# Kernel tuning notes

Measured on AMD Instinct MI355X. Metric: run time of the kernel, lower is better.

Reference implementation:

```python
import jax, jax.numpy as jnp
import numpy as np

B, N, E, HID, ED, NH = 2, 10000, 160000, 128, 32, 8
HD = HID // NH  # head_dim = 16
EPS = 1e-5


def setup_inputs() -> dict:
    key = jax.random.key(0)
    ks = jax.random.split(key, 12)
    s = 0.05  # keep pre-tanh activations in a sane range
    return {
        "h": jax.random.normal(ks[0], (B, N, HID), jnp.float32),
        "edge_attr": jax.random.normal(ks[1], (B, E, ED), jnp.float32),
        "edge_index": jax.random.randint(ks[2], (E, 2), 0, N),
        "Wq": jax.random.normal(ks[3], (HID, HID), jnp.float32) * s,
        "bq": jnp.zeros((HID,), jnp.float32),
        "Wk": jax.random.normal(ks[4], (HID, HID), jnp.float32) * s,
        "bk": jnp.zeros((HID,), jnp.float32),
        "Wv": jax.random.normal(ks[5], (HID, HID), jnp.float32) * s,
        "bv": jnp.zeros((HID,), jnp.float32),
        "We": jax.random.normal(ks[6], (HID, ED), jnp.float32) * s,
        "be": jnp.zeros((HID,), jnp.float32),
        "attn_vec": jax.random.normal(ks[7], (NH, HD), jnp.float32) * 0.02,
        "Ws": jax.random.normal(ks[8], (HID, HID), jnp.float32) * s,
        "bs": jnp.zeros((HID,), jnp.float32),
        "Wa": jax.random.normal(ks[9], (HID, HID), jnp.float32) * s,
        "ba": jnp.zeros((HID,), jnp.float32),
        "ln_g": jnp.ones((HID,), jnp.float32),
        "ln_b": jnp.zeros((HID,), jnp.float32),
    }


def reference(h, edge_attr, edge_index, Wq, bq, Wk, bk, Wv, bv, We, be,
              attn_vec, Ws, bs, Wa, ba, ln_g, ln_b):
    src = edge_index[:, 0]
    dst = edge_index[:, 1]
    b, n, hid = h.shape
    e_cnt = src.shape[0]

    h_src = h[:, src, :]  # [B,E,HID]
    h_dst = h[:, dst, :]

    q = (h_dst @ Wq.T + bq).reshape(b, e_cnt, NH, HD)
    k = (h_src @ Wk.T + bk).reshape(b, e_cnt, NH, HD)
    v = (h_src @ Wv.T + bv).reshape(b, e_cnt, NH, HD)
    e = (edge_attr @ We.T + be).reshape(b, e_cnt, NH, HD)

    # GATv2-style scores: [B,E,NH]
    logits = jnp.einsum('behd,hd->beh', jnp.tanh(q + k + e), attn_vec)
    logits = logits / np.float32(np.sqrt(HD))

    # segment softmax over edges grouped by dst node (stable)
    lt = jnp.transpose(logits, (1, 0, 2))  # [E,B,NH]
    mx = jax.ops.segment_max(lt, dst, num_segments=n)  # [N,B,NH]
    ex = jnp.exp(lt - mx[dst])
    den = jax.ops.segment_sum(ex, dst, num_segments=n)
    alpha = jnp.transpose(ex / den[dst], (1, 0, 2))  # [B,E,NH]

    msg = (alpha[..., None] * (v + e)).reshape(b, e_cnt, hid)  # [B,E,HID]
    agg = jax.ops.segment_sum(jnp.transpose(msg, (1, 0, 2)), dst, num_segments=n)
    agg = jnp.transpose(agg, (1, 0, 2))  # [B,N,HID]

    update = (h @ Ws.T + bs) + (agg @ Wa.T + ba)
    x = h + jax.nn.gelu(update, approximate=False)  # dropout is identity in eval

    mu = jnp.mean(x, axis=-1, keepdims=True)
    var = jnp.var(x, axis=-1, keepdims=True)
    return (x - mu) / jnp.sqrt(var + EPS) * ln_g + ln_b
```

## Files before the change

kernel.cpp:

```cpp
#include <hip/hip_runtime.h>
#include <math.h>
#include <stdint.h>

#define B_   2
#define N_   10000
#define E_   160000
#define HID_ 128
#define ED_  32
#define NH_  8
#define HD_  16
#define ROWS_ (B_ * N_)

using half2_t = __attribute__((ext_vector_type(2))) _Float16;

__device__ __forceinline__ half2_t f2h2(float a, float b) {
    return __builtin_bit_cast(half2_t, __builtin_amdgcn_cvt_pkrtz(a, b));
}
__device__ __forceinline__ uint32_t pkh2(float a, float b) {
    return __builtin_bit_cast(uint32_t, __builtin_amdgcn_cvt_pkrtz(a, b));
}


__global__ void zero_kernel(int* __restrict__ deg, int* __restrict__ cursor, int n) {
    int i = blockIdx.x * 256 + threadIdx.x;
    if (i < n) { deg[i] = 0; cursor[i] = 0; }
}

__global__ void hist_kernel(const int* __restrict__ ei, int* __restrict__ deg, int E) {
    int e = blockIdx.x * 256 + threadIdx.x;
    if (e < E) atomicAdd(&deg[ei[2 * e + 1]], 1);
}

__global__ __launch_bounds__(256) void scan_kernel(const int* __restrict__ deg,
                                                   int* __restrict__ off, int N) {
    __shared__ int sums[256];
    int t = threadIdx.x;
    int chunk = (N + 255) / 256;
    int s0 = t * chunk, s1 = min(N, s0 + chunk);
    int s = 0;
    for (int i = s0; i < s1; ++i) s += deg[i];
    sums[t] = s;
    __syncthreads();
    if (t == 0) {
        int run = 0;
        for (int i = 0; i < 256; ++i) { int v = sums[i]; sums[i] = run; run += v; }
        off[N] = run;
    }
    __syncthreads();
    int run = sums[t];
    for (int i = s0; i < s1; ++i) { off[i] = run; run += deg[i]; }
}

__global__ void fill_kernel(const int* __restrict__ ei, const int* __restrict__ off,
                            int* __restrict__ cursor, int* __restrict__ csr, int E) {
    int e = blockIdx.x * 256 + threadIdx.x;
    if (e < E) {
        int d = ei[2 * e + 1];
        int p = atomicAdd(&cursor[d], 1);
        csr[off[d] + p] = e;
    }
}


#define R_T 32
#define JC2 64
#define LDH2 68

__global__ __launch_bounds__(256) void qkvs_kernel(
    const float* __restrict__ h,
    const float* __restrict__ Wq, const float* __restrict__ bq,
    const float* __restrict__ Wk, const float* __restrict__ bk,
    const float* __restrict__ Wv, const float* __restrict__ bv,
    const float* __restrict__ Ws, const float* __restrict__ bs,
    const float* __restrict__ ba,
    float* __restrict__ Q, float* __restrict__ KV, float* __restrict__ S)
{
    __shared__ uint32_t hs[R_T * LDH2];
    __shared__ uint32_t wsm[JC2 * LDH2];
    __shared__ float bsm[512];

    int tid = threadIdx.x;
    int row0 = blockIdx.x * R_T;

    for (int f = tid; f < 512; f += 256) {
        float v;
        if (f < 128) v = bq[f];
        else if (f < 256) v = bk[f - 128];
        else if (f < 384) v = bv[f - 256];
        else v = bs[f - 384] + ba[f - 384];
        bsm[f] = v;
    }

    for (int f = tid; f < R_T * 32; f += 256) {
        int r = f >> 5, c4 = f & 31;
        float4 hv = *(const float4*)(h + (long)(row0 + r) * HID_ + c4 * 4);
        hs[r * LDH2 + c4 * 2]     = pkh2(hv.x, hv.y);
        hs[r * LDH2 + c4 * 2 + 1] = pkh2(hv.z, hv.w);
    }

    int rg = tid & 15;
    int cg = tid >> 4;

    for (int jc = 0; jc < 8; ++jc) {
        __syncthreads();
        for (int f = tid; f < JC2 * 32; f += 256) {
            int jr = f >> 5, c4 = f & 31;
            int J = jc * JC2 + jr;
            const float* Wp;
            if (J < 128)      Wp = Wq + (long)J * HID_;
            else if (J < 256) Wp = Wk + (long)(J - 128) * HID_;
            else if (J < 384) Wp = Wv + (long)(J - 256) * HID_;
            else              Wp = Ws + (long)(J - 384) * HID_;
            float4 wv = *(const float4*)(Wp + c4 * 4);
            wsm[jr * LDH2 + c4 * 2]     = pkh2(wv.x, wv.y);
            wsm[jr * LDH2 + c4 * 2 + 1] = pkh2(wv.z, wv.w);
        }
        __syncthreads();

        float acc[2][4];
        #pragma unroll
        for (int r = 0; r < 2; ++r)
            #pragma unroll
            for (int m = 0; m < 4; ++m) acc[r][m] = 0.f;

        #pragma unroll 4
        for (int kk = 0; kk < 16; ++kk) {
            const half2_t* h0 = (const half2_t*)(hs + rg * LDH2 + kk * 4);
            const half2_t* h1 = (const half2_t*)(hs + (rg + 16) * LDH2 + kk * 4);
            const half2_t* w0 = (const half2_t*)(wsm + cg * LDH2 + kk * 4);
            const half2_t* w1 = (const half2_t*)(wsm + (cg + 16) * LDH2 + kk * 4);
            const half2_t* w2 = (const half2_t*)(wsm + (cg + 32) * LDH2 + kk * 4);
            const half2_t* w3 = (const half2_t*)(wsm + (cg + 48) * LDH2 + kk * 4);
            #pragma unroll
            for (int d = 0; d < 4; ++d) {
                half2_t a0 = h0[d], a1 = h1[d];
                half2_t b0 = w0[d], b1 = w1[d], b2 = w2[d], b3 = w3[d];
                acc[0][0] = __builtin_amdgcn_fdot2(a0, b0, acc[0][0], false);
                acc[0][1] = __builtin_amdgcn_fdot2(a0, b1, acc[0][1], false);
                acc[0][2] = __builtin_amdgcn_fdot2(a0, b2, acc[0][2], false);
                acc[0][3] = __builtin_amdgcn_fdot2(a0, b3, acc[0][3], false);
                acc[1][0] = __builtin_amdgcn_fdot2(a1, b0, acc[1][0], false);
                acc[1][1] = __builtin_amdgcn_fdot2(a1, b1, acc[1][1], false);
                acc[1][2] = __builtin_amdgcn_fdot2(a1, b2, acc[1][2], false);
                acc[1][3] = __builtin_amdgcn_fdot2(a1, b3, acc[1][3], false);
            }
        }

        #pragma unroll
        for (int r = 0; r < 2; ++r) {
            long row = row0 + rg + r * 16;
            #pragma unroll
            for (int m = 0; m < 4; ++m) {
                int J = jc * JC2 + cg + m * 16;
                float v = acc[r][m] + bsm[J];
                if (J < 128)      Q[row * 128 + J] = v;
                else if (J < 256) KV[row * 256 + 2 * (J - 128)] = v;
                else if (J < 384) KV[row * 256 + 2 * (J - 256) + 1] = v;
                else              S[row * 128 + (J - 384)] = v;
            }
        }
    }
}

__global__ __launch_bounds__(256) void wa_kernel(
    const float* __restrict__ X, const float* __restrict__ Wa, float* __restrict__ A)
{
    __shared__ uint32_t hs[R_T * LDH2];
    __shared__ uint32_t wsm[JC2 * LDH2];

    int tid = threadIdx.x;
    int row0 = blockIdx.x * R_T;

    for (int f = tid; f < R_T * 32; f += 256) {
        int r = f >> 5, c4 = f & 31;
        float4 hv = *(const float4*)(X + (long)(row0 + r) * HID_ + c4 * 4);
        hs[r * LDH2 + c4 * 2]     = pkh2(hv.x, hv.y);
        hs[r * LDH2 + c4 * 2 + 1] = pkh2(hv.z, hv.w);
    }

    int rg = tid & 15;
    int cg = tid >> 4;

    for (int jc = 0; jc < 2; ++jc) {
        __syncthreads();
        for (int f = tid; f < JC2 * 32; f += 256) {
            int jr = f >> 5, c4 = f & 31;
            int J = jc * JC2 + jr;
            float4 wv = *(const float4*)(Wa + (long)J * HID_ + c4 * 4);
            wsm[jr * LDH2 + c4 * 2]     = pkh2(wv.x, wv.y);
            wsm[jr * LDH2 + c4 * 2 + 1] = pkh2(wv.z, wv.w);
        }
        __syncthreads();

        float acc[2][4];
        #pragma unroll
        for (int r = 0; r < 2; ++r)
            #pragma unroll
            for (int m = 0; m < 4; ++m) acc[r][m] = 0.f;

        #pragma unroll 4
        for (int kk = 0; kk < 16; ++kk) {
            const half2_t* h0 = (const half2_t*)(hs + rg * LDH2 + kk * 4);
            const half2_t* h1 = (const half2_t*)(hs + (rg + 16) * LDH2 + kk * 4);
            const half2_t* w0 = (const half2_t*)(wsm + cg * LDH2 + kk * 4);
            const half2_t* w1 = (const half2_t*)(wsm + (cg + 16) * LDH2 + kk * 4);
            const half2_t* w2 = (const half2_t*)(wsm + (cg + 32) * LDH2 + kk * 4);
            const half2_t* w3 = (const half2_t*)(wsm + (cg + 48) * LDH2 + kk * 4);
            #pragma unroll
            for (int d = 0; d < 4; ++d) {
                half2_t a0 = h0[d], a1 = h1[d];
                half2_t b0 = w0[d], b1 = w1[d], b2 = w2[d], b3 = w3[d];
                acc[0][0] = __builtin_amdgcn_fdot2(a0, b0, acc[0][0], false);
                acc[0][1] = __builtin_amdgcn_fdot2(a0, b1, acc[0][1], false);
                acc[0][2] = __builtin_amdgcn_fdot2(a0, b2, acc[0][2], false);
                acc[0][3] = __builtin_amdgcn_fdot2(a0, b3, acc[0][3], false);
                acc[1][0] = __builtin_amdgcn_fdot2(a1, b0, acc[1][0], false);
                acc[1][1] = __builtin_amdgcn_fdot2(a1, b1, acc[1][1], false);
                acc[1][2] = __builtin_amdgcn_fdot2(a1, b2, acc[1][2], false);
                acc[1][3] = __builtin_amdgcn_fdot2(a1, b3, acc[1][3], false);
            }
        }

        #pragma unroll
        for (int r = 0; r < 2; ++r) {
            long row = row0 + rg + r * 16;
            #pragma unroll
            for (int m = 0; m < 4; ++m) {
                int J = jc * JC2 + cg + m * 16;
                A[row * 128 + J] = acc[r][m];
            }
        }
    }
}


template <int CTRL>
__device__ __forceinline__ float dpp_add(float x) {
    int y = __builtin_amdgcn_mov_dpp(__float_as_int(x), CTRL, 0xF, 0xF, true);
    return x + __int_as_float(y);
}
__device__ __forceinline__ float hsum16(float p) {
    p = dpp_add<0xB1>(p);
    p = dpp_add<0x4E>(p);
    p = dpp_add<0x141>(p);
    p = dpp_add<0x140>(p);
    return p;
}


#define NPB 4
#define CHUNK 96
#define EAS 20

__global__ __launch_bounds__(128) void node_kernel(
    const float* __restrict__ edge_attr, const int* __restrict__ ei,
    const float* __restrict__ Q, const float* __restrict__ KV,
    const float* __restrict__ We, const float* __restrict__ be,
    const float* __restrict__ attn_vec,
    const int* __restrict__ off, const int* __restrict__ csr,
    float* __restrict__ agg)
{
    int n0 = blockIdx.x * NPB;
    int b  = blockIdx.y;
    int j  = threadIdx.x;
    long bN = (long)b * N_;

    __shared__ int sL[CHUNK];
    __shared__ uint32_t eaL[CHUNK * EAS];

    half2_t we16[16];
    {
        const float4* We4 = (const float4*)(We + (long)j * ED_);
        #pragma unroll
        for (int c = 0; c < 8; ++c) {
            float4 w = We4[c];
            we16[2 * c]     = f2h2(w.x, w.y);
            we16[2 * c + 1] = f2h2(w.z, w.w);
        }
    }
    float bej = be[j];
    float avj = attn_vec[j];

    float q0 = Q[(bN + n0 + 0) * 128 + j];
    float q1 = Q[(bN + n0 + 1) * 128 + j];
    float q2 = Q[(bN + n0 + 2) * 128 + j];
    float q3 = Q[(bN + n0 + 3) * 128 + j];

    int o0 = off[n0];
    int c1 = off[n0 + 1] - o0, c2 = off[n0 + 2] - o0,
        c3 = off[n0 + 3] - o0, c4_ = off[n0 + 4] - o0;
    int total = c4_;

    const float* eab = edge_attr + (long)b * E_ * ED_;
    const float* KVb = KV + bN * 256;

    float acc0 = 0.f, den0 = 0.f, acc1 = 0.f, den1 = 0.f;
    float acc2 = 0.f, den2 = 0.f, acc3 = 0.f, den3 = 0.f;

    auto edge_body = [&](int i, float qg, float& accg, float& deng) {
        int s = sL[i];
        float2 kv = *(const float2*)(KVb + (long)s * 256 + 2 * j);
        float ej = bej;
        const half2_t* ea = (const half2_t*)(eaL + i * EAS);
        #pragma unroll
        for (int c = 0; c < 16; ++c)
            ej = __builtin_amdgcn_fdot2(we16[c], ea[c], ej, false);
        float y = qg + kv.x + ej;
        float t = 1.f - 2.f * __builtin_amdgcn_rcpf(__expf(2.f * y) + 1.f);
        float p = hsum16(t * avj);
        float ex = __expf(p * 0.25f);
        deng += ex;
        accg += ex * (kv.y + ej);
    };

    auto range_loop = [&](int lo, int hi, float qg, float& accg, float& deng) {
        int i = lo;
        for (; i + 3 < hi; i += 4) {
            edge_body(i, qg, accg, deng);
            edge_body(i + 1, qg, accg, deng);
            edge_body(i + 2, qg, accg, deng);
            edge_body(i + 3, qg, accg, deng);
        }
        for (; i < hi; ++i) edge_body(i, qg, accg, deng);
    };

    for (int tau = 0; tau < total; tau += CHUNK) {
        int rows = min(total - tau, CHUNK);
        __syncthreads();
        for (int t = j; t < rows; t += 128) {
            int e = csr[o0 + tau + t];
            sL[t] = ei[2 * e];
        }
        for (int idx = j; idx < rows * 8; idx += 128) {
            int r = idx >> 3, c = idx & 7;
            int e = csr[o0 + tau + r];
            float4 f = *(const float4*)(eab + (long)e * ED_ + c * 4);
            eaL[r * EAS + c * 2]     = pkh2(f.x, f.y);
            eaL[r * EAS + c * 2 + 1] = pkh2(f.z, f.w);
        }
        __syncthreads();

        range_loop(max(0 - tau, 0),   min(c1 - tau, rows), q0, acc0, den0);
        range_loop(max(c1 - tau, 0),  min(c2 - tau, rows), q1, acc1, den1);
        range_loop(max(c2 - tau, 0),  min(c3 - tau, rows), q2, acc2, den2);
        range_loop(max(c3 - tau, 0),  min(c4_ - tau, rows), q3, acc3, den3);
    }

    agg[(bN + n0 + 0) * 128 + j] = (c1 > 0)   ? acc0 * __builtin_amdgcn_rcpf(den0) : 0.f;
    agg[(bN + n0 + 1) * 128 + j] = (c2 > c1)  ? acc1 * __builtin_amdgcn_rcpf(den1) : 0.f;
    agg[(bN + n0 + 2) * 128 + j] = (c3 > c2)  ? acc2 * __builtin_amdgcn_rcpf(den2) : 0.f;
    agg[(bN + n0 + 3) * 128 + j] = (c4_ > c3) ? acc3 * __builtin_amdgcn_rcpf(den3) : 0.f;
}


__global__ __launch_bounds__(128) void final_kernel(
    const float* __restrict__ h, const float* __restrict__ S, const float* __restrict__ A,
    const float* __restrict__ ln_g, const float* __restrict__ ln_b,
    float* __restrict__ out)
{
    long row = blockIdx.x;
    int j = threadIdx.x;
    __shared__ float red[4];

    float upd = S[row * 128 + j] + A[row * 128 + j];
    float ge = 0.5f * upd * (1.f + erff(upd * 0.70710678118654752f));
    float x = h[row * 128 + j] + ge;

    float s = x, s2 = x * x;
    #pragma unroll
    for (int m = 1; m < 64; m <<= 1) { s += __shfl_xor(s, m); s2 += __shfl_xor(s2, m); }
    int wv = j >> 6;
    if ((j & 63) == 0) { red[wv] = s; red[2 + wv] = s2; }
    __syncthreads();
    float Sm = red[0] + red[1], S2m = red[2] + red[3];
    float mu = Sm * (1.f / 128.f);
    float var = S2m * (1.f / 128.f) - mu * mu;
    out[row * 128 + j] = (x - mu) * rsqrtf(var + 1e-5f) * ln_g[j] + ln_b[j];
}


extern "C" void kernel_launch(void* const* d_in, const int* in_sizes, int n_in,
                              void* d_out, int out_size, void* d_ws, size_t ws_size,
                              hipStream_t stream) {
    const float* h         = (const float*)d_in[0];
    const float* edge_attr = (const float*)d_in[1];
    const int*   ei        = (const int*)  d_in[2];
    const float* Wq = (const float*)d_in[3];
    const float* bq = (const float*)d_in[4];
    const float* Wk = (const float*)d_in[5];
    const float* bk = (const float*)d_in[6];
    const float* Wv = (const float*)d_in[7];
    const float* bv = (const float*)d_in[8];
    const float* We = (const float*)d_in[9];
    const float* be = (const float*)d_in[10];
    const float* attn_vec = (const float*)d_in[11];
    const float* Ws = (const float*)d_in[12];
    const float* bs = (const float*)d_in[13];
    const float* Wa = (const float*)d_in[14];
    const float* ba = (const float*)d_in[15];
    const float* ln_g = (const float*)d_in[16];
    const float* ln_b = (const float*)d_in[17];
    float* out = (float*)d_out;

    size_t p = 0;
    auto alloc = [&](size_t bytes) { size_t r = p; p += (bytes + 255) & ~(size_t)255; return r; };
    char* ws = (char*)d_ws;
    float* Q    = (float*)(ws + alloc((size_t)ROWS_ * 128 * 4));
    float* KV   = (float*)(ws + alloc((size_t)ROWS_ * 256 * 4));
    float* S    = (float*)(ws + alloc((size_t)ROWS_ * 128 * 4));
    float* agg  = (float*)(ws + alloc((size_t)ROWS_ * 128 * 4));
    int* deg    = (int*)(ws + alloc((size_t)N_ * 4));
    int* cursor = (int*)(ws + alloc((size_t)N_ * 4));
    int* off    = (int*)(ws + alloc((size_t)(N_ + 1) * 4));
    int* csr    = (int*)(ws + alloc((size_t)E_ * 4));
    float* A = Q;
    (void)ws_size;

    zero_kernel<<<(N_ + 255) / 256, 256, 0, stream>>>(deg, cursor, N_);
    hist_kernel<<<(E_ + 255) / 256, 256, 0, stream>>>(ei, deg, E_);
    scan_kernel<<<1, 256, 0, stream>>>(deg, off, N_);
    fill_kernel<<<(E_ + 255) / 256, 256, 0, stream>>>(ei, off, cursor, csr, E_);

    qkvs_kernel<<<ROWS_ / R_T, 256, 0, stream>>>(h, Wq, bq, Wk, bk, Wv, bv, Ws, bs, ba,
                                                 Q, KV, S);

    dim3 grid(N_ / NPB, B_);
    node_kernel<<<grid, 128, 0, stream>>>(edge_attr, ei, Q, KV, We, be, attn_vec,
                                          off, csr, agg);

    wa_kernel<<<ROWS_ / R_T, 256, 0, stream>>>(agg, Wa, A);

    final_kernel<<<ROWS_, 128, 0, stream>>>(h, S, A, ln_g, ln_b, out);
}
```

Measured before the change: 206.1 us.

## Compute edge-attr projection per chunk with MFMA into shared memory

```diff
diff --git a/kernel.cpp b/kernel.cpp
--- a/kernel.cpp
+++ b/kernel.cpp
@@ -12,6 +12,8 @@
 #define ROWS_ (B_ * N_)
 
 using half2_t = __attribute__((ext_vector_type(2))) _Float16;
+using f16x8   = __attribute__((ext_vector_type(8))) _Float16;
+using f32x4   = __attribute__((ext_vector_type(4))) float;
 
 __device__ __forceinline__ half2_t f2h2(float a, float b) {
     return __builtin_bit_cast(half2_t, __builtin_amdgcn_cvt_pkrtz(a, b));
@@ -249,8 +251,9 @@
 
 
 #define NPB 4
-#define CHUNK 96
+#define CHUNK 64
 #define EAS 20
+#define PSTR 132
 
 __global__ __launch_bounds__(128) void node_kernel(
     const float* __restrict__ edge_attr, const int* __restrict__ ei,
@@ -263,22 +266,33 @@
     int n0 = blockIdx.x * NPB;
     int b  = blockIdx.y;
     int j  = threadIdx.x;
+    int lane = j & 63;
+    int wv = j >> 6;
     long bN = (long)b * N_;
 
     __shared__ int sL[CHUNK];
-    __shared__ uint32_t eaL[CHUNK * EAS];
-
-    half2_t we16[16];
+    __shared__ uint32_t eaF[CHUNK * EAS];
+    __shared__ _Float16 P16[CHUNK * PSTR];
+
+    f16x8 bfr[8];
+    float beC[8];
     {
-        const float4* We4 = (const float4*)(We + (long)j * ED_);
-        #pragma unroll
-        for (int c = 0; c < 8; ++c) {
-            float4 w = We4[c];
-            we16[2 * c]     = f2h2(w.x, w.y);
-            we16[2 * c + 1] = f2h2(w.z, w.w);
-        }
-    }
-    float bej = be[j];
+        int wrow = lane & 15;
+        int k0 = (lane >> 4) * 8;
+        #pragma unroll
+        for (int nt = 0; nt < 8; ++nt) {
+            const float* Wr = We + (long)(nt * 16 + wrow) * ED_ + k0;
+            float4 w0 = *(const float4*)(Wr);
+            float4 w1 = *(const float4*)(Wr + 4);
+            union { f16x8 v; uint32_t u[4]; } bu;
+            bu.u[0] = pkh2(w0.x, w0.y);
+            bu.u[1] = pkh2(w0.z, w0.w);
+            bu.u[2] = pkh2(w1.x, w1.y);
+            bu.u[3] = pkh2(w1.z, w1.w);
+            bfr[nt] = bu.v;
+            beC[nt] = be[nt * 16 + wrow];
+        }
+    }
     float avj = attn_vec[j];
 
     float q0 = Q[(bN + n0 + 0) * 128 + j];
@@ -300,11 +314,7 @@
     auto edge_body = [&](int i, float qg, float& accg, float& deng) {
         int s = sL[i];
         float2 kv = *(const float2*)(KVb + (long)s * 256 + 2 * j);
-        float ej = bej;
-        const half2_t* ea = (const half2_t*)(eaL + i * EAS);
-        #pragma unroll
-        for (int c = 0; c < 16; ++c)
-            ej = __builtin_amdgcn_fdot2(we16[c], ea[c], ej, false);
+        float ej = (float)P16[i * PSTR + j];
         float y = qg + kv.x + ej;
         float t = 1.f - 2.f * __builtin_amdgcn_rcpf(__expf(2.f * y) + 1.f);
         float p = hsum16(t * avj);
@@ -335,8 +345,29 @@
             int r = idx >> 3, c = idx & 7;
             int e = csr[o0 + tau + r];
             float4 f = *(const float4*)(eab + (long)e * ED_ + c * 4);
-            eaL[r * EAS + c * 2]     = pkh2(f.x, f.y);
-            eaL[r * EAS + c * 2 + 1] = pkh2(f.z, f.w);
+            uint2 pk;
+            pk.x = pkh2(f.x, f.y);
+            pk.y = pkh2(f.z, f.w);
+            *(uint2*)(&eaF[r * EAS + 2 * c]) = pk;
+        }
+        __syncthreads();
+
+        #pragma unroll
+        for (int m = 0; m < 2; ++m) {
+            int mt = wv * 2 + m;
+            int arow = mt * 16 + (lane & 15);
+            const f16x8 a = *(const f16x8*)(eaF + arow * EAS + (lane >> 4) * 4);
+            int prow = mt * 16 + (lane >> 4) * 4;
+            #pragma unroll
+            for (int nt = 0; nt < 8; ++nt) {
+                f32x4 cfr = { beC[nt], beC[nt], beC[nt], beC[nt] };
+                f32x4 d = __builtin_amdgcn_mfma_f32_16x16x32_f16(a, bfr[nt], cfr, 0, 0, 0);
+                int pcol = nt * 16 + (lane & 15);
+                P16[(prow + 0) * PSTR + pcol] = (_Float16)d[0];
+                P16[(prow + 1) * PSTR + pcol] = (_Float16)d[1];
+                P16[(prow + 2) * PSTR + pcol] = (_Float16)d[2];
+                P16[(prow + 3) * PSTR + pcol] = (_Float16)d[3];
+            }
         }
         __syncthreads();
 
```

Result: slower. 212.2 us (+2.9%).

## Use MFMA 16x16x32 f16 for node-wise QKVS and Wa projections

Applied to the files above, without the earlier changes.

```diff
diff --git a/kernel.cpp b/kernel.cpp
--- a/kernel.cpp
+++ b/kernel.cpp
@@ -12,6 +12,8 @@
 #define ROWS_ (B_ * N_)
 
 using half2_t = __attribute__((ext_vector_type(2))) _Float16;
+using f16x8   = __attribute__((ext_vector_type(8))) _Float16;
+using f32x4   = __attribute__((ext_vector_type(4))) float;
 
 __device__ __forceinline__ half2_t f2h2(float a, float b) {
     return __builtin_bit_cast(half2_t, __builtin_amdgcn_cvt_pkrtz(a, b));
@@ -62,9 +64,8 @@
 }
 
 
-#define R_T 32
-#define JC2 64
-#define LDH2 68
+#define GM 64
+#define LDA 68
 
 __global__ __launch_bounds__(256) void qkvs_kernel(
     const float* __restrict__ h,
@@ -75,84 +76,75 @@
     const float* __restrict__ ba,
     float* __restrict__ Q, float* __restrict__ KV, float* __restrict__ S)
 {
-    __shared__ uint32_t hs[R_T * LDH2];
-    __shared__ uint32_t wsm[JC2 * LDH2];
-    __shared__ float bsm[512];
+    __shared__ uint32_t As[GM * LDA];
+    __shared__ uint32_t Bs[128 * LDA];
+    __shared__ float bsm[128];
 
     int tid = threadIdx.x;
-    int row0 = blockIdx.x * R_T;
-
-    for (int f = tid; f < 512; f += 256) {
+    int lane = tid & 63;
+    int wave = tid >> 6;
+    int row0 = blockIdx.x * GM;
+    int J0 = blockIdx.y * 128;
+
+    if (tid < 128) {
+        int J = J0 + tid;
         float v;
-        if (f < 128) v = bq[f];
-        else if (f < 256) v = bk[f - 128];
-        else if (f < 384) v = bv[f - 256];
-        else v = bs[f - 384] + ba[f - 384];
-        bsm[f] = v;
-    }
-
-    for (int f = tid; f < R_T * 32; f += 256) {
+        if (J < 128)      v = bq[J];
+        else if (J < 256) v = bk[J - 128];
+        else if (J < 384) v = bv[J - 256];
+        else              v = bs[J - 384] + ba[J - 384];
+        bsm[tid] = v;
+    }
+
+    for (int f = tid; f < GM * 32; f += 256) {
         int r = f >> 5, c4 = f & 31;
-        float4 hv = *(const float4*)(h + (long)(row0 + r) * HID_ + c4 * 4);
-        hs[r * LDH2 + c4 * 2]     = pkh2(hv.x, hv.y);
-        hs[r * LDH2 + c4 * 2 + 1] = pkh2(hv.z, hv.w);
-    }
-
-    int rg = tid & 15;
-    int cg = tid >> 4;
-
-    for (int jc = 0; jc < 8; ++jc) {
-        __syncthreads();
-        for (int f = tid; f < JC2 * 32; f += 256) {
-            int jr = f >> 5, c4 = f & 31;
-            int J = jc * JC2 + jr;
-            const float* Wp;
-            if (J < 128)      Wp = Wq + (long)J * HID_;
-            else if (J < 256) Wp = Wk + (long)(J - 128) * HID_;
-            else if (J < 384) Wp = Wv + (long)(J - 256) * HID_;
-            else              Wp = Ws + (long)(J - 384) * HID_;
-            float4 wv = *(const float4*)(Wp + c4 * 4);
-            wsm[jr * LDH2 + c4 * 2]     = pkh2(wv.x, wv.y);
-            wsm[jr * LDH2 + c4 * 2 + 1] = pkh2(wv.z, wv.w);
-        }
-        __syncthreads();
-
-        float acc[2][4];
-        #pragma unroll
-        for (int r = 0; r < 2; ++r)
-            #pragma unroll
-            for (int m = 0; m < 4; ++m) acc[r][m] = 0.f;
-
-        #pragma unroll 4
-        for (int kk = 0; kk < 16; ++kk) {
-            const half2_t* h0 = (const half2_t*)(hs + rg * LDH2 + kk * 4);
-            const half2_t* h1 = (const half2_t*)(hs + (rg + 16) * LDH2 + kk * 4);
-            const half2_t* w0 = (const half2_t*)(wsm + cg * LDH2 + kk * 4);
-            const half2_t* w1 = (const half2_t*)(wsm + (cg + 16) * LDH2 + kk * 4);
-            const half2_t* w2 = (const half2_t*)(wsm + (cg + 32) * LDH2 + kk * 4);
-            const half2_t* w3 = (const half2_t*)(wsm + (cg + 48) * LDH2 + kk * 4);
-            #pragma unroll
-            for (int d = 0; d < 4; ++d) {
-                half2_t a0 = h0[d], a1 = h1[d];
-                half2_t b0 = w0[d], b1 = w1[d], b2 = w2[d], b3 = w3[d];
-                acc[0][0] = __builtin_amdgcn_fdot2(a0, b0, acc[0][0], false);
-                acc[0][1] = __builtin_amdgcn_fdot2(a0, b1, acc[0][1], false);
-                acc[0][2] = __builtin_amdgcn_fdot2(a0, b2, acc[0][2], false);
-                acc[0][3] = __builtin_amdgcn_fdot2(a0, b3, acc[0][3], false);
-                acc[1][0] = __builtin_amdgcn_fdot2(a1, b0, acc[1][0], false);
-                acc[1][1] = __builtin_amdgcn_fdot2(a1, b1, acc[1][1], false);
-                acc[1][2] = __builtin_amdgcn_fdot2(a1, b2, acc[1][2], false);
-                acc[1][3] = __builtin_amdgcn_fdot2(a1, b3, acc[1][3], false);
-            }
-        }
-
-        #pragma unroll
-        for (int r = 0; r < 2; ++r) {
-            long row = row0 + rg + r * 16;
-            #pragma unroll
-            for (int m = 0; m < 4; ++m) {
-                int J = jc * JC2 + cg + m * 16;
-                float v = acc[r][m] + bsm[J];
+        long row = row0 + r;
+        float4 hv = (row < ROWS_) ? *(const float4*)(h + row * HID_ + c4 * 4)
+                                  : make_float4(0.f, 0.f, 0.f, 0.f);
+        As[r * LDA + c4 * 2]     = pkh2(hv.x, hv.y);
+        As[r * LDA + c4 * 2 + 1] = pkh2(hv.z, hv.w);
+    }
+    for (int f = tid; f < 128 * 32; f += 256) {
+        int jr = f >> 5, c4 = f & 31;
+        int J = J0 + jr;
+        const float* Wp;
+        if (J < 128)      Wp = Wq + (long)J * HID_;
+        else if (J < 256) Wp = Wk + (long)(J - 128) * HID_;
+        else if (J < 384) Wp = Wv + (long)(J - 256) * HID_;
+        else              Wp = Ws + (long)(J - 384) * HID_;
+        float4 wv = *(const float4*)(Wp + c4 * 4);
+        Bs[jr * LDA + c4 * 2]     = pkh2(wv.x, wv.y);
+        Bs[jr * LDA + c4 * 2 + 1] = pkh2(wv.z, wv.w);
+    }
+    __syncthreads();
+
+    f32x4 acc[8];
+    #pragma unroll
+    for (int nt = 0; nt < 8; ++nt) {
+        float c = bsm[nt * 16 + (lane & 15)];
+        acc[nt] = (f32x4){ c, c, c, c };
+    }
+
+    int ar = wave * 16 + (lane & 15);
+    #pragma unroll
+    for (int ks = 0; ks < 4; ++ks) {
+        f16x8 a = *(const f16x8*)(As + ar * LDA + ks * 16 + (lane >> 4) * 4);
+        #pragma unroll
+        for (int nt = 0; nt < 8; ++nt) {
+            f16x8 b = *(const f16x8*)(Bs + (nt * 16 + (lane & 15)) * LDA + ks * 16 + (lane >> 4) * 4);
+            acc[nt] = __builtin_amdgcn_mfma_f32_16x16x32_f16(a, b, acc[nt], 0, 0, 0);
+        }
+    }
+
+    #pragma unroll
+    for (int nt = 0; nt < 8; ++nt) {
+        int J = J0 + nt * 16 + (lane & 15);
+        long rbase = row0 + wave * 16 + (lane >> 4) * 4;
+        #pragma unroll
+        for (int r = 0; r < 4; ++r) {
+            long row = rbase + r;
+            if (row < ROWS_) {
+                float v = acc[nt][r];
                 if (J < 128)      Q[row * 128 + J] = v;
                 else if (J < 256) KV[row * 256 + 2 * (J - 128)] = v;
                 else if (J < 384) KV[row * 256 + 2 * (J - 256) + 1] = v;
@@ -165,70 +157,53 @@
 __global__ __launch_bounds__(256) void wa_kernel(
     const float* __restrict__ X, const float* __restrict__ Wa, float* __restrict__ A)
 {
-    __shared__ uint32_t hs[R_T * LDH2];
-    __shared__ uint32_t wsm[JC2 * LDH2];
+    __shared__ uint32_t As[GM * LDA];
+    __shared__ uint32_t Bs[128 * LDA];
 
     int tid = threadIdx.x;
-    int row0 = blockIdx.x * R_T;
-
-    for (int f = tid; f < R_T * 32; f += 256) {
+    int lane = tid & 63;
+    int wave = tid >> 6;
+    int row0 = blockIdx.x * GM;
+
+    for (int f = tid; f < GM * 32; f += 256) {
         int r = f >> 5, c4 = f & 31;
-        float4 hv = *(const float4*)(X + (long)(row0 + r) * HID_ + c4 * 4);
-        hs[r * LDH2 + c4 * 2]     = pkh2(hv.x, hv.y);
-        hs[r * LDH2 + c4 * 2 + 1] = pkh2(hv.z, hv.w);
-    }
-
-    int rg = tid & 15;
-    int cg = tid >> 4;
-
-    for (int jc = 0; jc < 2; ++jc) {
-        __syncthreads();
-        for (int f = tid; f < JC2 * 32; f += 256) {
-            int jr = f >> 5, c4 = f & 31;
-            int J = jc * JC2 + jr;
-            float4 wv = *(const float4*)(Wa + (long)J * HID_ + c4 * 4);
-            wsm[jr * LDH2 + c4 * 2]     = pkh2(wv.x, wv.y);
-            wsm[jr * LDH2 + c4 * 2 + 1] = pkh2(wv.z, wv.w);
-        }
-        __syncthreads();
-
-        float acc[2][4];
-        #pragma unroll
-        for (int r = 0; r < 2; ++r)
-            #pragma unroll
-            for (int m = 0; m < 4; ++m) acc[r][m] = 0.f;
-
-        #pragma unroll 4
-        for (int kk = 0; kk < 16; ++kk) {
-            const half2_t* h0 = (const half2_t*)(hs + rg * LDH2 + kk * 4);
-            const half2_t* h1 = (const half2_t*)(hs + (rg + 16) * LDH2 + kk * 4);
-            const half2_t* w0 = (const half2_t*)(wsm + cg * LDH2 + kk * 4);
-            const half2_t* w1 = (const half2_t*)(wsm + (cg + 16) * LDH2 + kk * 4);
-            const half2_t* w2 = (const half2_t*)(wsm + (cg + 32) * LDH2 + kk * 4);
-            const half2_t* w3 = (const half2_t*)(wsm + (cg + 48) * LDH2 + kk * 4);
-            #pragma unroll
-            for (int d = 0; d < 4; ++d) {
-                half2_t a0 = h0[d], a1 = h1[d];
-                half2_t b0 = w0[d], b1 = w1[d], b2 = w2[d], b3 = w3[d];
-                acc[0][0] = __builtin_amdgcn_fdot2(a0, b0, acc[0][0], false);
-                acc[0][1] = __builtin_amdgcn_fdot2(a0, b1, acc[0][1], false);
-                acc[0][2] = __builtin_amdgcn_fdot2(a0, b2, acc[0][2], false);
-                acc[0][3] = __builtin_amdgcn_fdot2(a0, b3, acc[0][3], false);
-                acc[1][0] = __builtin_amdgcn_fdot2(a1, b0, acc[1][0], false);
-                acc[1][1] = __builtin_amdgcn_fdot2(a1, b1, acc[1][1], false);
-                acc[1][2] = __builtin_amdgcn_fdot2(a1, b2, acc[1][2], false);
-                acc[1][3] = __builtin_amdgcn_fdot2(a1, b3, acc[1][3], false);
-            }
-        }
-
-        #pragma unroll
-        for (int r = 0; r < 2; ++r) {
-            long row = row0 + rg + r * 16;
-            #pragma unroll
-            for (int m = 0; m < 4; ++m) {
-                int J = jc * JC2 + cg + m * 16;
-                A[row * 128 + J] = acc[r][m];
-            }
+        long row = row0 + r;
+        float4 hv = (row < ROWS_) ? *(const float4*)(X + row * HID_ + c4 * 4)
+                                  : make_float4(0.f, 0.f, 0.f, 0.f);
+        As[r * LDA + c4 * 2]     = pkh2(hv.x, hv.y);
+        As[r * LDA + c4 * 2 + 1] = pkh2(hv.z, hv.w);
+    }
+    for (int f = tid; f < 128 * 32; f += 256) {
+        int jr = f >> 5, c4 = f & 31;
+        float4 wv = *(const float4*)(Wa + (long)jr * HID_ + c4 * 4);
+        Bs[jr * LDA + c4 * 2]     = pkh2(wv.x, wv.y);
+        Bs[jr * LDA + c4 * 2 + 1] = pkh2(wv.z, wv.w);
+    }
+    __syncthreads();
+
+    f32x4 acc[8];
+    #pragma unroll
+    for (int nt = 0; nt < 8; ++nt) acc[nt] = (f32x4){ 0.f, 0.f, 0.f, 0.f };
+
+    int ar = wave * 16 + (lane & 15);
+    #pragma unroll
+    for (int ks = 0; ks < 4; ++ks) {
+        f16x8 a = *(const f16x8*)(As + ar * LDA + ks * 16 + (lane >> 4) * 4);
+        #pragma unroll
+        for (int nt = 0; nt < 8; ++nt) {
+            f16x8 b = *(const f16x8*)(Bs + (nt * 16 + (lane & 15)) * LDA + ks * 16 + (lane >> 4) * 4);
+            acc[nt] = __builtin_amdgcn_mfma_f32_16x16x32_f16(a, b, acc[nt], 0, 0, 0);
+        }
+    }
+
+    #pragma unroll
+    for (int nt = 0; nt < 8; ++nt) {
+        int J = nt * 16 + (lane & 15);
+        long rbase = row0 + wave * 16 + (lane >> 4) * 4;
+        #pragma unroll
+        for (int r = 0; r < 4; ++r) {
+            long row = rbase + r;
+            if (row < ROWS_) A[row * 128 + J] = acc[nt][r];
         }
     }
 }
@@ -335,8 +310,8 @@
             int r = idx >> 3, c = idx & 7;
             int e = csr[o0 + tau + r];
             float4 f = *(const float4*)(eab + (long)e * ED_ + c * 4);
-            eaL[r * EAS + c * 2]     = pkh2(f.x, f.y);
-            eaL[r * EAS + c * 2 + 1] = pkh2(f.z, f.w);
+            eaL[r * EAS + 2 * c]     = pkh2(f.x, f.y);
+            eaL[r * EAS + 2 * c + 1] = pkh2(f.z, f.w);
         }
         __syncthreads();
 
@@ -421,14 +396,16 @@
     scan_kernel<<<1, 256, 0, stream>>>(deg, off, N_);
     fill_kernel<<<(E_ + 255) / 256, 256, 0, stream>>>(ei, off, cursor, csr, E_);
 
-    qkvs_kernel<<<ROWS_ / R_T, 256, 0, stream>>>(h, Wq, bq, Wk, bk, Wv, bv, Ws, bs, ba,
-                                                 Q, KV, S);
+    dim3 ggrid((ROWS_ + GM - 1) / GM, 4);
+    qkvs_kernel<<<ggrid, 256, 0, stream>>>(h, Wq, bq, Wk, bk, Wv, bv, Ws, bs, ba,
+                                           Q, KV, S);
 
     dim3 grid(N_ / NPB, B_);
     node_kernel<<<grid, 128, 0, stream>>>(edge_attr, ei, Q, KV, We, be, attn_vec,
                                           off, csr, agg);
 
-    wa_kernel<<<ROWS_ / R_T, 256, 0, stream>>>(agg, Wa, A);
+    dim3 wgrid((ROWS_ + GM - 1) / GM, 1);
+    wa_kernel<<<wgrid, 256, 0, stream>>>(agg, Wa, A);
 
     final_kernel<<<ROWS_, 128, 0, stream>>>(h, S, A, ln_g, ln_b, out);
 }
```

Result: faster. 176.6 us (-14.3%).
